# Performance work log

Hardware: AMD Instinct MI355X
Metric: run time of the kernel (lower is better)

## Reference

```python
import jax, jax.numpy as jnp
import numpy as np

KH = KW = 3
PAD = 1

def _patches(x):
    # x: [B, C, H, W] -> periodic pad then 3x3 patches [B, C, KH, KW, H, W]
    B, C, H, W = x.shape
    xp = jnp.pad(x, ((0, 0), (0, 0), (PAD, PAD), (PAD, PAD)), mode='wrap')
    rows = []
    for i in range(KH):
        cols = [xp[:, :, i:i + H, j:j + W] for j in range(KW)]
        rows.append(jnp.stack(cols, axis=2))  # [B, C, KW, H, W]
    return jnp.stack(rows, axis=2)  # [B, C, KH, KW, H, W]

def setup_inputs() -> dict:
    key = jax.random.key(0)
    k1, k2, k3 = jax.random.split(key, 3)
    B, C, O, H, W = 16, 64, 64, 128, 128
    input = jax.random.normal(k1, (B, C, H, W), dtype=jnp.float32)
    weight = jax.random.normal(k2, (B, C * KH * KW, O), dtype=jnp.float32) * 0.05
    bias = jax.random.normal(k3, (B, O), dtype=jnp.float32) * 0.05
    return {"input": input, "weight": weight, "bias": bias}

def reference(input, weight, bias):
    B, C, H, W = input.shape
    O = weight.shape[-1]
    p = _patches(input)  # [B, C, KH, KW, H, W]
    w = weight.reshape(B, C, KH, KW, O)
    # per-sample dynamic conv: contract over (C, KH, KW)
    y = jnp.einsum('bcijhw,bcijo->bohw', p, w)
    return y + bias[:, :, None, None]
```

## Files before the change

### kernel.cpp

```cpp
#include <hip/hip_runtime.h>
#include <stdint.h>

#define B_N 16
#define C_N 64
#define O_N 64
#define H_N 128
#define W_N 128

typedef short bf16x8 __attribute__((ext_vector_type(8)));
typedef float f32x4 __attribute__((ext_vector_type(4)));
typedef unsigned short u16;
typedef u16 u16x4 __attribute__((ext_vector_type(4)));

__device__ __forceinline__ u16 f2bf(float f) {
    uint32_t u = __float_as_uint(f);
    u += 0x7FFFu + ((u >> 16) & 1u);
    return (u16)(u >> 16);
}

__device__ __forceinline__ int swz(int w) { return (w & 7) << 4; }

__global__ __launch_bounds__(256) void prep_weights(const float* __restrict__ wt,
                                                    u16* __restrict__ wf) {
    int idx = blockIdx.x * 256 + threadIdx.x;
    int e = idx;
    int o4 = e & 15; e >>= 4;
    int ij = e % 9;  e /= 9;
    int c  = e & 63; e >>= 6;
    int b  = e;
    f32x4 v = *reinterpret_cast<const f32x4*>(
        wt + ((size_t)b * 576 + (size_t)c * 9 + ij) * 64 + o4 * 4);
    const int cs = c >> 5, lgc = (c >> 3) & 3, j8 = c & 7;
#pragma unroll
    for (int k = 0; k < 4; ++k) {
        int o = o4 * 4 + k;
        int of = o >> 4, lrc = o & 15;
        size_t dst = ((size_t)((((b * 9 + ij) * 2 + cs) * 4 + of) * 64 + lgc * 16 + lrc)) * 8 + j8;
        wf[dst] = f2bf(v[k]);
    }
}

__global__ __launch_bounds__(512, 2) void conv_main(const float* __restrict__ x,
                                                    const u16* __restrict__ wf,
                                                    const float* __restrict__ bias,
                                                    float* __restrict__ y) {
    __shared__ u16 xl[6 * 128 * 64];

    const int lid = (blockIdx.x & 7) * 32 + (blockIdx.x >> 3);
    const int b   = lid >> 4;
    const int h0  = (lid & 15) * 8;
    const int tid = threadIdx.x;
    const int wid = tid >> 6;
    const int l   = tid & 63;
    const int wave_m = wid >> 1;
    const int wave_n = wid & 1;
    const int m0 = wave_m * 32;
    const int o0 = wave_n * 32;
    const int lr = l & 15;
    const int lg = l >> 4;

    const int w4 = tid & 31;
    const int cq = tid >> 5;
    const float* xb = x + (size_t)b * (64 * 128 * 128);
    const u16* wfb  = wf + (size_t)b * 36864;

    auto ldrow = [&](int s, f32x4* d) {
        int hr = (h0 + s + 127) & 127;
        const float* src = xb + ((size_t)cq * 4 * 128 + hr) * 128 + w4 * 4;
        d[0] = *reinterpret_cast<const f32x4*>(src);
        d[1] = *reinterpret_cast<const f32x4*>(src + 16384);
        d[2] = *reinterpret_cast<const f32x4*>(src + 32768);
        d[3] = *reinterpret_cast<const f32x4*>(src + 49152);
    };
    auto wrrow = [&](int slot, const f32x4* d) {
#pragma unroll
        for (int j = 0; j < 4; ++j) {
            int w = w4 * 4 + j;
            u16x4 pk;
            pk.x = f2bf(d[0][j]); pk.y = f2bf(d[1][j]);
            pk.z = f2bf(d[2][j]); pk.w = f2bf(d[3][j]);
            int byte = slot * 16384 + w * 128 + cq * 8;
            byte ^= swz(w);
            *reinterpret_cast<u16x4*>(reinterpret_cast<char*>(xl) + byte) = pk;
        }
    };

    f32x4 s0[4], s1[4], s2[4], st[4];
    ldrow(0, s0); ldrow(1, s1); ldrow(2, s2);

    bf16x8 wreg[9][2][2];
#pragma unroll
    for (int ij = 0; ij < 9; ++ij)
#pragma unroll
        for (int cs = 0; cs < 2; ++cs)
#pragma unroll
            for (int nf = 0; nf < 2; ++nf)
                wreg[ij][cs][nf] = *reinterpret_cast<const bf16x8*>(
                    wfb + (size_t)(((ij * 2 + cs) * 4 + wave_n * 2 + nf) * 64 + l) * 8);

    const float bv0 = bias[b * 64 + o0 + lr];
    const float bv1 = bias[b * 64 + o0 + 16 + lr];

    wrrow(0, s0); wrrow(1, s1); wrrow(2, s2);
    ldrow(3, s0); ldrow(4, st);
    wrrow(3, s0);
    __syncthreads();

    int slA = 0;
#pragma unroll 1
    for (int r = 0; r < 8; ++r) {
        const int slB = (slA + 1 == 6) ? 0 : slA + 1;
        const int slC = (slB + 1 == 6) ? 0 : slB + 1;
        const int slW = (slC + 2 >= 6) ? slC + 2 - 6 : slC + 2;
        const int base0 = slA * 16384, base1 = slB * 16384, base2 = slC * 16384;

        f32x4 acc[2][2];
#pragma unroll
        for (int mf = 0; mf < 2; ++mf)
#pragma unroll
            for (int nf = 0; nf < 2; ++nf)
                acc[mf][nf] = (f32x4){0.f, 0.f, 0.f, 0.f};

#pragma unroll
        for (int ij = 0; ij < 9; ++ij) {
            if (ij == 0 && r < 6) wrrow(slW, st);
            if (ij == 3 && r < 5) ldrow(r + 5, st);

            const int i = ij / 3;
            const int jsh = ij % 3 - 1;
            const int rbase = (i == 0) ? base0 : (i == 1) ? base1 : base2;
#pragma unroll
            for (int cs = 0; cs < 2; ++cs) {
                const int cb = cs * 64 + lg * 16;
                bf16x8 afr[2];
#pragma unroll
                for (int mf = 0; mf < 2; ++mf) {
                    int w = (m0 + mf * 16 + lr + jsh + 128) & 127;
                    int byte = rbase + w * 128 + cb;
                    byte ^= swz(w);
                    afr[mf] = *reinterpret_cast<const bf16x8*>(
                        reinterpret_cast<const char*>(xl) + byte);
                }
#pragma unroll
                for (int mf = 0; mf < 2; ++mf) {
                    acc[mf][0] = __builtin_amdgcn_mfma_f32_16x16x32_bf16(afr[mf], wreg[ij][cs][0], acc[mf][0], 0, 0, 0);
                    acc[mf][1] = __builtin_amdgcn_mfma_f32_16x16x32_bf16(afr[mf], wreg[ij][cs][1], acc[mf][1], 0, 0, 0);
                }
            }
        }

        const int h = h0 + r;
#pragma unroll
        for (int nf = 0; nf < 2; ++nf) {
            int o = o0 + nf * 16 + lr;
            float bv = nf ? bv1 : bv0;
#pragma unroll
            for (int mf = 0; mf < 2; ++mf) {
                int w0 = m0 + mf * 16 + lg * 4;
                float* dst = y + (((size_t)b * 64 + o) * 128 + h) * 128 + w0;
                f32x4 out;
                out[0] = acc[mf][nf][0] + bv;
                out[1] = acc[mf][nf][1] + bv;
                out[2] = acc[mf][nf][2] + bv;
                out[3] = acc[mf][nf][3] + bv;
                *reinterpret_cast<f32x4*>(dst) = out;
            }
        }

        if ((r & 1) && r < 7) __syncthreads();
        slA = slB;
    }
}

__global__ void naive_conv(const float* __restrict__ x, const float* __restrict__ wt,
                           const float* __restrict__ bias, float* __restrict__ y) {
    int w = threadIdx.x;
    int h = blockIdx.x & 127;
    int o = (blockIdx.x >> 7) & 63;
    int b = blockIdx.x >> 13;
    float s = bias[b * 64 + o];
    for (int c = 0; c < 64; ++c)
        for (int i = 0; i < 3; ++i)
            for (int j = 0; j < 3; ++j) {
                int hh = (h + i + 127) & 127;
                int ww = (w + j + 127) & 127;
                s += x[(((size_t)b * 64 + c) * 128 + hh) * 128 + ww] *
                     wt[((size_t)b * 576 + (size_t)(c * 9 + i * 3 + j)) * 64 + o];
            }
    y[(((size_t)b * 64 + o) * 128 + h) * 128 + w] = s;
}

extern "C" void kernel_launch(void* const* d_in, const int* in_sizes, int n_in,
                              void* d_out, int out_size, void* d_ws, size_t ws_size,
                              hipStream_t stream) {
    const float* x    = (const float*)d_in[0];
    const float* wt   = (const float*)d_in[1];
    const float* bias = (const float*)d_in[2];
    float* y = (float*)d_out;

    const size_t WF_ELEMS = (size_t)B_N * 9 * 2 * 4 * 64 * 8;
    const size_t WF_BYTES = WF_ELEMS * sizeof(u16);

    if (ws_size >= WF_BYTES) {
        u16* wf = (u16*)d_ws;
        hipLaunchKernelGGL(prep_weights, dim3(576), dim3(256), 0, stream, wt, wf);
        hipLaunchKernelGGL(conv_main, dim3(B_N * H_N / 8), dim3(512), 0, stream, x, wf, bias, y);
    } else {
        hipLaunchKernelGGL(naive_conv, dim3(B_N * O_N * H_N), dim3(128), 0, stream, x, wt, bias, y);
    }
}
```

Baseline: 38.30 us.

## Fuse weight bf16 conversion into conv kernel via shared memory staging

Removes the separate prep_weights launch and the workspace round-trip. Each block now converts its sample's fp32 weights to bf16 and writes them in MFMA fragment layout into the LDS buffer, then loads the per-wave register fragments from LDS before the buffer is reused for input rows. The cost is redundant conversion work: all 16 blocks of a sample each read and convert the same 147KB of weights, plus two extra barriers in the prologue. The naive fallback path is also dropped.

After: 37.11 us. 1.03x faster.

```diff
diff --git a/kernel.cpp b/kernel.cpp
--- a/kernel.cpp
+++ b/kernel.cpp
@@ -20,28 +20,8 @@
 
 __device__ __forceinline__ int swz(int w) { return (w & 7) << 4; }
 
-__global__ __launch_bounds__(256) void prep_weights(const float* __restrict__ wt,
-                                                    u16* __restrict__ wf) {
-    int idx = blockIdx.x * 256 + threadIdx.x;
-    int e = idx;
-    int o4 = e & 15; e >>= 4;
-    int ij = e % 9;  e /= 9;
-    int c  = e & 63; e >>= 6;
-    int b  = e;
-    f32x4 v = *reinterpret_cast<const f32x4*>(
-        wt + ((size_t)b * 576 + (size_t)c * 9 + ij) * 64 + o4 * 4);
-    const int cs = c >> 5, lgc = (c >> 3) & 3, j8 = c & 7;
-#pragma unroll
-    for (int k = 0; k < 4; ++k) {
-        int o = o4 * 4 + k;
-        int of = o >> 4, lrc = o & 15;
-        size_t dst = ((size_t)((((b * 9 + ij) * 2 + cs) * 4 + of) * 64 + lgc * 16 + lrc)) * 8 + j8;
-        wf[dst] = f2bf(v[k]);
-    }
-}
-
 __global__ __launch_bounds__(512, 2) void conv_main(const float* __restrict__ x,
-                                                    const u16* __restrict__ wf,
+                                                    const float* __restrict__ wt,
                                                     const float* __restrict__ bias,
                                                     float* __restrict__ y) {
     __shared__ u16 xl[6 * 128 * 64];
@@ -61,8 +41,8 @@
 
     const int w4 = tid & 31;
     const int cq = tid >> 5;
-    const float* xb = x + (size_t)b * (64 * 128 * 128);
-    const u16* wfb  = wf + (size_t)b * 36864;
+    const float* xb  = x  + (size_t)b * (64 * 128 * 128);
+    const float* wtb = wt + (size_t)b * (576 * 64);
 
     auto ldrow = [&](int s, f32x4* d) {
         int hr = (h0 + s + 127) & 127;
@@ -79,14 +59,32 @@
             u16x4 pk;
             pk.x = f2bf(d[0][j]); pk.y = f2bf(d[1][j]);
             pk.z = f2bf(d[2][j]); pk.w = f2bf(d[3][j]);
-            int byte = slot * 16384 + w * 128 + cq * 8;
-            byte ^= swz(w);
+            int byte = slot * 16384 + w * 128 + ((cq * 8) ^ swz(w));
             *reinterpret_cast<u16x4*>(reinterpret_cast<char*>(xl) + byte) = pk;
         }
     };
 
+    u16* wl = xl;
+#pragma unroll
+    for (int it = 0; it < 18; ++it) {
+        int task = it * 512 + tid;
+        int o4 = task & 15;
+        int t2 = task >> 4;
+        int ij = t2 % 9;
+        int c  = t2 / 9;
+        f32x4 v = *reinterpret_cast<const f32x4*>(wtb + ((size_t)c * 9 + ij) * 64 + o4 * 4);
+        const int cs = c >> 5, lgc = (c >> 3) & 3, j8 = c & 7;
+#pragma unroll
+        for (int k = 0; k < 4; ++k) {
+            int o = o4 * 4 + k;
+            int of = o >> 4, lrc = o & 15;
+            wl[(((ij * 2 + cs) * 4 + of) * 64 + lgc * 16 + lrc) * 8 + j8] = f2bf(v[k]);
+        }
+    }
+
     f32x4 s0[4], s1[4], s2[4], st[4];
     ldrow(0, s0); ldrow(1, s1); ldrow(2, s2);
+    __syncthreads();
 
     bf16x8 wreg[9][2][2];
 #pragma unroll
@@ -96,10 +94,11 @@
 #pragma unroll
             for (int nf = 0; nf < 2; ++nf)
                 wreg[ij][cs][nf] = *reinterpret_cast<const bf16x8*>(
-                    wfb + (size_t)(((ij * 2 + cs) * 4 + wave_n * 2 + nf) * 64 + l) * 8);
+                    wl + (size_t)(((ij * 2 + cs) * 4 + wave_n * 2 + nf) * 64 + l) * 8);
 
     const float bv0 = bias[b * 64 + o0 + lr];
     const float bv1 = bias[b * 64 + o0 + 16 + lr];
+    __syncthreads();
 
     wrrow(0, s0); wrrow(1, s1); wrrow(2, s2);
     ldrow(3, s0); ldrow(4, st);
@@ -136,8 +135,7 @@
 #pragma unroll
                 for (int mf = 0; mf < 2; ++mf) {
                     int w = (m0 + mf * 16 + lr + jsh + 128) & 127;
-                    int byte = rbase + w * 128 + cb;
-                    byte ^= swz(w);
+                    int byte = rbase + w * 128 + (cb ^ swz(w));
                     afr[mf] = *reinterpret_cast<const bf16x8*>(
                         reinterpret_cast<const char*>(xl) + byte);
                 }
@@ -172,24 +170,6 @@
     }
 }
 
-__global__ void naive_conv(const float* __restrict__ x, const float* __restrict__ wt,
-                           const float* __restrict__ bias, float* __restrict__ y) {
-    int w = threadIdx.x;
-    int h = blockIdx.x & 127;
-    int o = (blockIdx.x >> 7) & 63;
-    int b = blockIdx.x >> 13;
-    float s = bias[b * 64 + o];
-    for (int c = 0; c < 64; ++c)
-        for (int i = 0; i < 3; ++i)
-            for (int j = 0; j < 3; ++j) {
-                int hh = (h + i + 127) & 127;
-                int ww = (w + j + 127) & 127;
-                s += x[(((size_t)b * 64 + c) * 128 + hh) * 128 + ww] *
-                     wt[((size_t)b * 576 + (size_t)(c * 9 + i * 3 + j)) * 64 + o];
-            }
-    y[(((size_t)b * 64 + o) * 128 + h) * 128 + w] = s;
-}
-
 extern "C" void kernel_launch(void* const* d_in, const int* in_sizes, int n_in,
                               void* d_out, int out_size, void* d_ws, size_t ws_size,
                               hipStream_t stream) {
@@ -197,15 +177,8 @@
     const float* wt   = (const float*)d_in[1];
     const float* bias = (const float*)d_in[2];
     float* y = (float*)d_out;
+    (void)d_ws; (void)ws_size;
 
-    const size_t WF_ELEMS = (size_t)B_N * 9 * 2 * 4 * 64 * 8;
-    const size_t WF_BYTES = WF_ELEMS * sizeof(u16);
-
-    if (ws_size >= WF_BYTES) {
-        u16* wf = (u16*)d_ws;
-        hipLaunchKernelGGL(prep_weights, dim3(576), dim3(256), 0, stream, wt, wf);
-        hipLaunchKernelGGL(conv_main, dim3(B_N * H_N / 8), dim3(512), 0, stream, x, wf, bias, y);
-    } else {
-        hipLaunchKernelGGL(naive_conv, dim3(B_N * O_N * H_N), dim3(128), 0, stream, x, wt, bias, y);
-    }
+    hipLaunchKernelGGL(conv_main, dim3(B_N * H_N / 8), dim3(512), 0, stream,
+                       x, wt, bias, y);
 }
```
